# Optimization experiments

Hardware: AMD Instinct MI355X
Metric: run time of the kernel (lower is better)

## Reference

```python
import jax, jax.numpy as jnp
import numpy as np

NEG_SLOPE = 0.02

def _leaky(x):
    return jnp.where(x >= 0, x, NEG_SLOPE * x)

def _conv1d(x, w, b):
    # x: (B, Cin, T), w: (Cout, Cin, 3) torch layout; SAME padding, stride 1
    y = jax.lax.conv_general_dilated(x, w, window_strides=(1,), padding=[(1, 1)],
                                     dimension_numbers=('NCH', 'OIH', 'NCH'))
    return y + b[None, :, None]

def setup_inputs() -> dict:
    key = jax.random.key(0)
    ks = iter(jax.random.split(key, 40))
    B, T, NA, S, NE, NID = 32768, 9, 64, 32, 53, 5000
    def rn(shape, scale=0.1):
        return (jax.random.normal(next(ks), shape, dtype=jnp.float32) * scale)
    inp = {
        'x': jax.random.normal(next(ks), (B, T, NA), dtype=jnp.float32),
        'identity_id': jax.random.randint(next(ks), (B,), 0, NID, dtype=jnp.int32),
        'cw1': rn((32, 64, 3)), 'cb1': rn((32,)),
        'cw2': rn((64, 32, 3)), 'cb2': rn((64,)),
        'cw3': rn((128, 64, 3)), 'cb3': rn((128,)),
        'cw4': rn((64, 128, 3)), 'cb4': rn((64,)),
        'fw1': rn((128, 64)), 'fb1': rn((128,)),
        'fw2': rn((64, 128)), 'fb2': rn((64,)),
        'fw3': rn((32, 64)), 'fb3': rn((32,)),
        'aw1': rn((16, 32, 3)), 'ab1': rn((16,)),
        'aw2': rn((8, 16, 3)), 'ab2': rn((8,)),
        'aw3': rn((4, 8, 3)), 'ab3': rn((4,)),
        'aw4': rn((2, 4, 3)), 'ab4': rn((2,)),
        'aw5': rn((1, 2, 3)), 'ab5': rn((1,)),
        'lw': rn((9, 9)), 'lb': rn((9,)),
        'mapping': jax.random.normal(next(ks), (1, NID, NE, S), dtype=jnp.float32),
    }
    return inp

def reference(x, identity_id, cw1, cb1, cw2, cb2, cw3, cb3, cw4, cb4,
              fw1, fb1, fw2, fb2, fw3, fb3,
              aw1, ab1, aw2, ab2, aw3, ab3, aw4, ab4, aw5, ab5,
              lw, lb, mapping):
    B, T, _ = x.shape          # (B, 9, 64)
    S = fw3.shape[0]           # subspace_dim = 32
    h = jnp.transpose(x, (0, 2, 1))  # (B, 64, 9)
    h = _leaky(_conv1d(h, cw1, cb1))
    h = _leaky(_conv1d(h, cw2, cb2))
    h = _leaky(_conv1d(h, cw3, cb3))
    h = _leaky(_conv1d(h, cw4, cb4))  # (B, 64, 9)
    # faithful to torch: reshape (B,64,9) -> (B*9, 1, 64) row-major (mixes C and T)
    h = h.reshape(B * T, 64)
    h = _leaky(h @ fw1.T + fb1)
    h = _leaky(h @ fw2.T + fb2)
    h = jnp.tanh(h @ fw3.T + fb3)        # (B*T, S)
    rs_T = h.reshape(B, T, S).transpose(0, 2, 1)  # (B, S, T)
    a = _leaky(_conv1d(rs_T, aw1, ab1))
    a = _leaky(_conv1d(a, aw2, ab2))
    a = _leaky(_conv1d(a, aw3, ab3))
    a = _leaky(_conv1d(a, aw4, ab4))
    a = _leaky(_conv1d(a, aw5, ab5))     # (B, 1, T)
    logits = a.reshape(B, T) @ lw.T + lb
    att = jax.nn.softmax(logits, axis=1)            # (B, T)
    sub = jnp.einsum('bst,bt->bs', rs_T, att)       # (B, S)
    m = mapping[0][identity_id]                     # (B, n_expression, S)
    return 10.0 * jnp.einsum('bes,bs->be', m, sub)  # (B, n_expression)
```

## Files before the change

### kernel.cpp

```cpp
#include <hip/hip_runtime.h>
#include <hip/hip_bf16.h>
#include <math.h>

#define THREADS 512
#define WAVES 8
#define NB 16

typedef __attribute__((ext_vector_type(8))) short bf16x8;
typedef __attribute__((ext_vector_type(4))) float f32x4;

__device__ __forceinline__ float leaky(float x){ return x >= 0.f ? x : 0.02f*x; }
__device__ __forceinline__ float fast_tanh(float x){
  float e = __expf(2.f*x);
  return 1.f - 2.f/(e + 1.f);
}

__device__ __forceinline__ unsigned short f2bf(float f){
  union { float f; unsigned u; } v; v.f = f;
  unsigned r = (v.u + 0x7FFFu + ((v.u >> 16) & 1u)) >> 16;
  return (unsigned short)r;
}
__device__ __forceinline__ float bf2f(unsigned short h){
  union { unsigned u; float f; } v; v.u = ((unsigned)h) << 16;
  return v.f;
}
__device__ __forceinline__ unsigned pack2bf(float a, float b){
  float2 t; t.x = a; t.y = b;
  __hip_bfloat162 h = __float22bfloat162_rn(t);
  union { __hip_bfloat162 h; unsigned u; } c; c.h = h;
  return c.u;
}

template<int L2R>
__device__ __forceinline__ unsigned swz(unsigned b){
  if constexpr (L2R < 0) return b;
  else return b ^ (((b >> L2R) & 7u) << 4);
}

__device__ __forceinline__ f32x4 mfma16(bf16x8 a, bf16x8 b, f32x4 c){
  return __builtin_amdgcn_mfma_f32_16x16x32_bf16(a, b, c, 0, 0, 0);
}

#define WB_C1 0
#define WB_C2 6144
#define WB_C3 12288
#define WB_C4 36864
#define WB_F1 61440
#define WB_F2 69632
#define WB_F3 77824
#define WB_A1 79872
#define WB_A2 81408
#define WB_A3 82432
#define WB_A4 82944
#define WB_A5 83456
#define WP_TOTAL 83968

__global__ void pack_weights(
    const float* __restrict__ cw1, const float* __restrict__ cw2,
    const float* __restrict__ cw3, const float* __restrict__ cw4,
    const float* __restrict__ fw1, const float* __restrict__ fw2,
    const float* __restrict__ fw3, const float* __restrict__ aw1,
    const float* __restrict__ aw2, const float* __restrict__ aw3,
    const float* __restrict__ aw4, const float* __restrict__ aw5,
    short* __restrict__ wp)
{
  int g = blockIdx.x*256 + threadIdx.x;
  if (g >= WP_TOTAL) return;
  const float* w; int base, l2cp, cinw, cout, KS; bool conv;
  if      (g < WB_C2){ w=cw1; base=WB_C1; l2cp=6; cinw=64;  cout=32;  KS=6;  conv=true; }
  else if (g < WB_C3){ w=cw2; base=WB_C2; l2cp=5; cinw=32;  cout=64;  KS=3;  conv=true; }
  else if (g < WB_C4){ w=cw3; base=WB_C3; l2cp=6; cinw=64;  cout=128; KS=6;  conv=true; }
  else if (g < WB_F1){ w=cw4; base=WB_C4; l2cp=7; cinw=128; cout=64;  KS=12; conv=true; }
  else if (g < WB_F2){ w=fw1; base=WB_F1; l2cp=6; cinw=64;  cout=128; KS=2;  conv=false; }
  else if (g < WB_F3){ w=fw2; base=WB_F2; l2cp=7; cinw=128; cout=64;  KS=4;  conv=false; }
  else if (g < WB_A1){ w=fw3; base=WB_F3; l2cp=6; cinw=64;  cout=32;  KS=2;  conv=false; }
  else if (g < WB_A2){ w=aw1; base=WB_A1; l2cp=5; cinw=32;  cout=16;  KS=3;  conv=true; }
  else if (g < WB_A3){ w=aw2; base=WB_A2; l2cp=4; cinw=16;  cout=8;   KS=2;  conv=true; }
  else if (g < WB_A4){ w=aw3; base=WB_A3; l2cp=3; cinw=8;   cout=4;   KS=1;  conv=true; }
  else if (g < WB_A5){ w=aw4; base=WB_A4; l2cp=3; cinw=4;   cout=2;   KS=1;  conv=true; }
  else               { w=aw5; base=WB_A5; l2cp=3; cinw=2;   cout=1;   KS=1;  conv=true; }
  int local = g - base;
  int frag = local >> 9;
  int lane = (local >> 3) & 63;
  int j    = local & 7;
  int nt = frag / KS, ks = frag - nt*KS;
  int hi = lane >> 4, lo = lane & 15;
  int k = ks*32 + hi*8 + j;
  int n = nt*16 + lo;
  float v = 0.f;
  if (n < cout){
    if (conv){
      int dt = k >> l2cp, ci = k & ((1<<l2cp)-1);
      if (dt < 3 && ci < cinw) v = w[((size_t)n*cinw + ci)*3 + dt];
    } else {
      v = w[(size_t)n*cinw + k];
    }
  }
  wp[g] = (short)f2bf(v);
}

template<int CINP, int CINW, int COUT, int STORE_CH, int KS, int MYNT,
         int L2RI, int L2RO, bool IN_CONV, int OUT_MODE, int ACT,
         int LBASE, bool PACKED>
__device__ __forceinline__ void mfma_layer(
    const short* __restrict__ wp, const float* __restrict__ w,
    const float* __restrict__ bias, const char* __restrict__ inb,
    char* __restrict__ outb, int tid)
{
  constexpr int NT = (COUT + 15)/16;
  constexpr int NTG = (NT + MYNT - 1)/MYNT;
  constexpr int L2CINP = (CINP==8?3:CINP==16?4:CINP==32?5:CINP==64?6:7);
  const int wave = tid >> 6, lane = tid & 63;
  const int hi = lane >> 4, lo = lane & 15;

  int nt0, mlo, mhi;
  if constexpr (NTG >= WAVES){
    nt0 = (wave % NTG) * MYNT; mlo = 0; mhi = 9;
  } else {
    constexpr int WPN = WAVES/NTG;
    int seg = wave / NTG; int g = wave - seg*NTG;
    nt0 = g*MYNT; mlo = (9*seg)/WPN; mhi = (9*(seg+1))/WPN;
  }

  bf16x8 Bf[MYNT][KS];
  #pragma unroll
  for (int nt = 0; nt < MYNT; ++nt){
    #pragma unroll
    for (int ks = 0; ks < KS; ++ks){
      if constexpr (PACKED){
        Bf[nt][ks] = *(const bf16x8*)(wp + LBASE + (((nt0+nt)*KS + ks) << 9) + lane*8);
      } else {
        int n = (nt0+nt)*16 + lo;
        #pragma unroll
        for (int j = 0; j < 8; ++j){
          int k = ks*32 + hi*8 + j;
          float v = 0.f;
          if (n < COUT){
            if constexpr (IN_CONV){
              int dt = k >> L2CINP, ci = k & (CINP-1);
              if (dt < 3 && ci < CINW) v = w[((size_t)n*CINW + ci)*3 + dt];
            } else {
              v = w[(size_t)n*CINP + k];
            }
          }
          Bf[nt][ks][j] = (short)f2bf(v);
        }
      }
    }
  }

  float bb[MYNT][4];
  #pragma unroll
  for (int nt = 0; nt < MYNT; ++nt){
    #pragma unroll
    for (int r = 0; r < 4; ++r){
      int n = (nt0+nt)*16 + hi*4 + r;
      bb[nt][r] = (n < COUT) ? bias[n] : 0.f;
    }
  }

  const unsigned hi16 = (unsigned)hi * 16u;

  for (int m = mlo; m < mhi; ++m){
    int R = m*16 + lo;
    int bl2 = 0, t2 = 0, ridx = R;
    if constexpr (IN_CONV || OUT_MODE != 1){
      bl2 = R/9; t2 = R - bl2*9; ridx = bl2*11 + t2;
    }
    unsigned base_in;
    if constexpr (IN_CONV) base_in = ((unsigned)ridx << (L2CINP+1));
    else                   base_in = ((unsigned)R    << (L2CINP+1));

    f32x4 acc[MYNT];
    #pragma unroll
    for (int nt = 0; nt < MYNT; ++nt)
      acc[nt] = (f32x4){bb[nt][0], bb[nt][1], bb[nt][2], bb[nt][3]};

    #pragma unroll
    for (int ks = 0; ks < KS; ++ks){
      unsigned byte0 = base_in + (unsigned)(ks*64) + hi16;
      bf16x8 Af = *(const bf16x8*)(inb + swz<L2RI>(byte0));
      #pragma unroll
      for (int nt = 0; nt < MYNT; ++nt)
        acc[nt] = mfma16(Bf[nt][ks], Af, acc[nt]);
    }

    #pragma unroll
    for (int nt = 0; nt < MYNT; ++nt){
      const int n0 = (nt0+nt)*16 + hi*4;
      if constexpr (OUT_MODE == 2){
        #pragma unroll
        for (int r = 0; r < 4; ++r){
          int n = n0 + r;
          float vr = (ACT==0) ? leaky(acc[nt][r]) : fast_tanh(acc[nt][r]);
          unsigned byte = (unsigned)((bl2*576 + n*9 + t2)*2);
          *(short*)(outb + swz<L2RO>(byte)) = (short)f2bf(vr);
        }
      } else if constexpr (STORE_CH == 1){
        if (hi == 0){
          float vr = (ACT==0) ? leaky(acc[nt][0]) : fast_tanh(acc[nt][0]);
          *(short*)(outb + (unsigned)((ridx + 1)*2)) = (short)f2bf(vr);
        }
      } else {
        if (n0 < STORE_CH){
          float v[4];
          #pragma unroll
          for (int r = 0; r < 4; ++r){
            float vr = (ACT==0) ? leaky(acc[nt][r]) : fast_tanh(acc[nt][r]);
            if constexpr (STORE_CH > COUT){ if (n0 + r >= COUT) vr = 0.f; }
            v[r] = vr;
          }
          unsigned rowO = (OUT_MODE == 1) ? (unsigned)R : (unsigned)(ridx + 1);
          unsigned byte = rowO * (unsigned)(STORE_CH*2) + (unsigned)(n0*2);
          uint2 pk; pk.x = pack2bf(v[0], v[1]); pk.y = pack2bf(v[2], v[3]);
          *(uint2*)(outb + swz<L2RO>(byte)) = pk;
        }
      }
    }
  }

  if constexpr (OUT_MODE == 0){
    for (int i = tid; i < NB*2*STORE_CH/4; i += THREADS){
      int bl = i / (2*STORE_CH/4); int rem = i - bl*(2*STORE_CH/4);
      int side = rem / (STORE_CH/4); int c4 = rem - side*(STORE_CH/4);
      unsigned byte = (unsigned)(((bl*11 + side*10)*STORE_CH + c4*4)*2);
      uint2 z; z.x = 0u; z.y = 0u;
      *(uint2*)(outb + swz<L2RO>(byte)) = z;
    }
  }
}

#define A2OFF 5760
#define A3OFF 8704
#define A4OFF 11648
#define A5OFF 14592

template<bool PACKED>
__global__ __launch_bounds__(THREADS, 4)
void fused_expr_kernel(
    const float* __restrict__ x, const int* __restrict__ ident,
    const float* __restrict__ cw1, const float* __restrict__ cb1,
    const float* __restrict__ cw2, const float* __restrict__ cb2,
    const float* __restrict__ cw3, const float* __restrict__ cb3,
    const float* __restrict__ cw4, const float* __restrict__ cb4,
    const float* __restrict__ fw1, const float* __restrict__ fb1,
    const float* __restrict__ fw2, const float* __restrict__ fb2,
    const float* __restrict__ fw3, const float* __restrict__ fb3,
    const float* __restrict__ aw1, const float* __restrict__ ab1,
    const float* __restrict__ aw2, const float* __restrict__ ab2,
    const float* __restrict__ aw3, const float* __restrict__ ab3,
    const float* __restrict__ aw4, const float* __restrict__ ab4,
    const float* __restrict__ aw5, const float* __restrict__ ab5,
    const float* __restrict__ lw,  const float* __restrict__ lb,
    const float* __restrict__ mapping, const short* __restrict__ wp,
    float* __restrict__ out)
{
  __shared__ __align__(16) char pool[67584];
  __shared__ float logits_s[NB*9];
  __shared__ float att_s[NB*9];
  __shared__ float sub_s[NB*32];

  char* RA = pool;
  char* RB = pool + 45056;

  const int tid = threadIdx.x;
  const int b0 = blockIdx.x * NB;
  const int p  = tid >> 4;
  const int bl = tid & 15;

  {
    const float4* xb4 = (const float4*)(x + (size_t)b0 * 576);
    for (int i = tid; i < NB*144; i += THREADS){
      int b = i / 144; int rem = i - b*144;
      int t = rem >> 4; int c4 = rem & 15;
      float4 v = xb4[i];
      uint2 pk;
      pk.x = pack2bf(v.x, v.y);
      pk.y = pack2bf(v.z, v.w);
      unsigned byte = (unsigned)(((b*11 + t + 1)*64 + c4*4)*2);
      *(uint2*)(RB + swz<7>(byte)) = pk;
    }
    for (int i = tid; i < 512; i += THREADS){
      int b = i >> 5; int rem = i & 31;
      int side = rem >> 4; int c4 = rem & 15;
      unsigned byte = (unsigned)(((b*11 + side*10)*64 + c4*4)*2);
      uint2 z; z.x = 0u; z.y = 0u;
      *(uint2*)(RB + swz<7>(byte)) = z;
    }
  }
  __syncthreads();

  mfma_layer<64, 64, 32, 32, 6, 2, 7, 6, true, 0, 0, WB_C1, PACKED>(wp, cw1, cb1, RB, RA, tid); __syncthreads();
  mfma_layer<32, 32, 64, 64, 3, 2, 6, 7, true, 0, 0, WB_C2, PACKED>(wp, cw2, cb2, RA, RB, tid); __syncthreads();
  mfma_layer<64, 64,128,128, 6, 2, 7, 8, true, 0, 0, WB_C3, PACKED>(wp, cw3, cb3, RB, RA, tid); __syncthreads();
  mfma_layer<128,128,64, 64,12, 1, 8, 7, true, 2, 0, WB_C4, PACKED>(wp, cw4, cb4, RA, RB, tid); __syncthreads();
  mfma_layer<64, 64,128,128, 2, 4, 7, 8, false,1, 0, WB_F1, PACKED>(wp, fw1, fb1, RB, RA, tid); __syncthreads();
  mfma_layer<128,128,64, 64, 4, 2, 8, 7, false,1, 0, WB_F2, PACKED>(wp, fw2, fb2, RA, RB, tid); __syncthreads();
  mfma_layer<64, 64, 32, 32, 2, 2, 7, 6, false,0, 1, WB_F3, PACKED>(wp, fw3, fb3, RB, RA, tid); __syncthreads();

  char* rs = RA;
  char* a1 = RB;
  char* a2 = RB + A2OFF;
  char* a3 = RB + A3OFF;
  char* a4 = RB + A4OFF;
  char* a5 = RB + A5OFF;

  mfma_layer<32, 32, 16, 16, 3, 1, 6, 5, true, 0, 0, WB_A1, PACKED>(wp, aw1, ab1, rs, a1, tid); __syncthreads();
  mfma_layer<16, 16,  8,  8, 2, 1, 5,-1, true, 0, 0, WB_A2, PACKED>(wp, aw2, ab2, a1, a2, tid); __syncthreads();
  mfma_layer< 8,  8,  4,  8, 1, 1,-1,-1, true, 0, 0, WB_A3, PACKED>(wp, aw3, ab3, a2, a3, tid); __syncthreads();
  mfma_layer< 8,  4,  2,  8, 1, 1,-1,-1, true, 0, 0, WB_A4, PACKED>(wp, aw4, ab4, a3, a4, tid); __syncthreads();
  mfma_layer< 8,  2,  1,  1, 1, 1,-1,-1, true, 3, 0, WB_A5, PACKED>(wp, aw5, ab5, a4, a5, tid); __syncthreads();

  if (p < 9){
    float acc = lb[p];
    #pragma unroll
    for (int t = 0; t < 9; ++t)
      acc = fmaf(lw[p*9 + t], bf2f(*(const unsigned short*)(a5 + (bl*11 + t + 1)*2)), acc);
    logits_s[bl*9 + p] = acc;
  }
  __syncthreads();

  if (p == 0){
    float m = -1e30f;
    #pragma unroll
    for (int t = 0; t < 9; ++t) m = fmaxf(m, logits_s[bl*9 + t]);
    float s = 0.f, ex[9];
    #pragma unroll
    for (int t = 0; t < 9; ++t){ ex[t] = __expf(logits_s[bl*9 + t] - m); s += ex[t]; }
    float inv = 1.f / s;
    #pragma unroll
    for (int t = 0; t < 9; ++t) att_s[bl*9 + t] = ex[t]*inv;
  }
  __syncthreads();

  {
    int s = p;
    float acc = 0.f;
    #pragma unroll
    for (int t = 0; t < 9; ++t){
      unsigned byte = (unsigned)(((bl*11 + t + 1)*32 + s)*2);
      acc = fmaf(bf2f(*(const unsigned short*)(rs + swz<6>(byte))), att_s[bl*9 + t], acc);
    }
    sub_s[bl*32 + s] = acc;
  }
  __syncthreads();

  {
    const int b = b0 + bl;
    const size_t id = (size_t)ident[b];
    const float* mb = mapping + id*53*32;
    float subv[32];
    #pragma unroll
    for (int s = 0; s < 32; ++s) subv[s] = sub_s[bl*32 + s];
    for (int e = p; e < 53; e += 32){
      const float4* mrow4 = (const float4*)(mb + e*32);
      float acc = 0.f;
      #pragma unroll
      for (int s4 = 0; s4 < 8; ++s4){
        float4 mv = mrow4[s4];
        acc = fmaf(mv.x, subv[s4*4+0], acc);
        acc = fmaf(mv.y, subv[s4*4+1], acc);
        acc = fmaf(mv.z, subv[s4*4+2], acc);
        acc = fmaf(mv.w, subv[s4*4+3], acc);
      }
      out[(size_t)b*53 + e] = 10.f*acc;
    }
  }
}

extern "C" void kernel_launch(void* const* d_in, const int* in_sizes, int n_in,
                              void* d_out, int out_size, void* d_ws, size_t ws_size,
                              hipStream_t stream) {
  const float* x    = (const float*)d_in[0];
  const int*   ident= (const int*)  d_in[1];
  const float* cw1  = (const float*)d_in[2];  const float* cb1 = (const float*)d_in[3];
  const float* cw2  = (const float*)d_in[4];  const float* cb2 = (const float*)d_in[5];
  const float* cw3  = (const float*)d_in[6];  const float* cb3 = (const float*)d_in[7];
  const float* cw4  = (const float*)d_in[8];  const float* cb4 = (const float*)d_in[9];
  const float* fw1  = (const float*)d_in[10]; const float* fb1 = (const float*)d_in[11];
  const float* fw2  = (const float*)d_in[12]; const float* fb2 = (const float*)d_in[13];
  const float* fw3  = (const float*)d_in[14]; const float* fb3 = (const float*)d_in[15];
  const float* aw1  = (const float*)d_in[16]; const float* ab1 = (const float*)d_in[17];
  const float* aw2  = (const float*)d_in[18]; const float* ab2 = (const float*)d_in[19];
  const float* aw3  = (const float*)d_in[20]; const float* ab3 = (const float*)d_in[21];
  const float* aw4  = (const float*)d_in[22]; const float* ab4 = (const float*)d_in[23];
  const float* aw5  = (const float*)d_in[24]; const float* ab5 = (const float*)d_in[25];
  const float* lw   = (const float*)d_in[26]; const float* lb  = (const float*)d_in[27];
  const float* mapping = (const float*)d_in[28];

  const int B = 32768;
  dim3 grid(B / NB), block(THREADS);

  const bool packed = ws_size >= (size_t)(WP_TOTAL * 2);
  short* wpk = (short*)d_ws;

  if (packed){
    pack_weights<<<dim3(WP_TOTAL/256), dim3(256), 0, stream>>>(
        cw1, cw2, cw3, cw4, fw1, fw2, fw3, aw1, aw2, aw3, aw4, aw5, wpk);
    fused_expr_kernel<true><<<grid, block, 0, stream>>>(
        x, ident, cw1, cb1, cw2, cb2, cw3, cb3, cw4, cb4,
        fw1, fb1, fw2, fb2, fw3, fb3,
        aw1, ab1, aw2, ab2, aw3, ab3, aw4, ab4, aw5, ab5,
        lw, lb, mapping, wpk, (float*)d_out);
  } else {
    fused_expr_kernel<false><<<grid, block, 0, stream>>>(
        x, ident, cw1, cb1, cw2, cb2, cw3, cb3, cw4, cb4,
        fw1, fb1, fw2, fb2, fw3, fb3,
        aw1, ab1, aw2, ab2, aw3, ab3, aw4, ab4, aw5, ab5,
        lw, lb, mapping, wpk, (float*)d_out);
  }
}
```

Baseline: 145.5 us.

## Halve batch per block, drop padded rows, and raise occupancy

Each block now handles 8 sequences instead of 16, and activations are stored densely (9 rows per sequence) rather than with padding rows. Conv boundaries are handled by masked A-fragment loads instead of explicitly zeroing pad rows. The shared-memory pool shrinks from about 66KB to about 30KB, and launch bounds now target 8 blocks per SM, so more blocks fit per CU. In exchange, per-tile MYNT drops to 1 in several layers, so each block reloads weights more often relative to its work, and the conditional loads add branches to the inner loop.

Measured after the change: 269.9 us. +85.5%, slower.

```diff
diff --git a/kernel.cpp b/kernel.cpp
--- a/kernel.cpp
+++ b/kernel.cpp
@@ -4,7 +4,14 @@
 
 #define THREADS 512
 #define WAVES 8
-#define NB 16
+#define NB 8
+#define MROWS (NB*9)
+#define MT 5
+
+#define P1OFF 0
+#define P2OFF 20480
+#define GUARD 256
+#define POOLSZ (20480+10240+GUARD)
 
 typedef __attribute__((ext_vector_type(8))) short bf16x8;
 typedef __attribute__((ext_vector_type(4))) float f32x4;
@@ -115,11 +122,11 @@
 
   int nt0, mlo, mhi;
   if constexpr (NTG >= WAVES){
-    nt0 = (wave % NTG) * MYNT; mlo = 0; mhi = 9;
+    nt0 = (wave % NTG)*MYNT; mlo = 0; mhi = MT;
   } else {
     constexpr int WPN = WAVES/NTG;
     int seg = wave / NTG; int g = wave - seg*NTG;
-    nt0 = g*MYNT; mlo = (9*seg)/WPN; mhi = (9*(seg+1))/WPN;
+    nt0 = g*MYNT; mlo = (MT*seg)/WPN; mhi = (MT*(seg+1))/WPN;
   }
 
   bf16x8 Bf[MYNT][KS];
@@ -159,17 +166,15 @@
     }
   }
 
-  const unsigned hi16 = (unsigned)hi * 16u;
+  const int k0h = hi*8;
 
   for (int m = mlo; m < mhi; ++m){
     int R = m*16 + lo;
-    int bl2 = 0, t2 = 0, ridx = R;
-    if constexpr (IN_CONV || OUT_MODE != 1){
-      bl2 = R/9; t2 = R - bl2*9; ridx = bl2*11 + t2;
-    }
-    unsigned base_in;
-    if constexpr (IN_CONV) base_in = ((unsigned)ridx << (L2CINP+1));
-    else                   base_in = ((unsigned)R    << (L2CINP+1));
+    int tl = 0;
+    if constexpr (IN_CONV){
+      int blr = (int)((unsigned)R/9u);
+      tl = R - blr*9;
+    }
 
     f32x4 acc[MYNT];
     #pragma unroll
@@ -178,8 +183,18 @@
 
     #pragma unroll
     for (int ks = 0; ks < KS; ++ks){
-      unsigned byte0 = base_in + (unsigned)(ks*64) + hi16;
-      bf16x8 Af = *(const bf16x8*)(inb + swz<L2RI>(byte0));
+      bf16x8 Af = {};
+      if constexpr (IN_CONV){
+        int k0 = ks*32 + k0h;
+        int dtv = k0 >> L2CINP;
+        if ((unsigned)(tl + dtv - 1) < 9u && dtv < 3){
+          unsigned byte0 = (unsigned)(((R-1) << (L2CINP+1)) + (k0 << 1));
+          Af = *(const bf16x8*)(inb + swz<L2RI>(byte0));
+        }
+      } else {
+        unsigned byte0 = (unsigned)((R << (L2CINP+1)) + (ks*32 + k0h)*2);
+        Af = *(const bf16x8*)(inb + swz<L2RI>(byte0));
+      }
       #pragma unroll
       for (int nt = 0; nt < MYNT; ++nt)
         acc[nt] = mfma16(Bf[nt][ks], Af, acc[nt]);
@@ -189,17 +204,19 @@
     for (int nt = 0; nt < MYNT; ++nt){
       const int n0 = (nt0+nt)*16 + hi*4;
       if constexpr (OUT_MODE == 2){
-        #pragma unroll
-        for (int r = 0; r < 4; ++r){
-          int n = n0 + r;
-          float vr = (ACT==0) ? leaky(acc[nt][r]) : fast_tanh(acc[nt][r]);
-          unsigned byte = (unsigned)((bl2*576 + n*9 + t2)*2);
-          *(short*)(outb + swz<L2RO>(byte)) = (short)f2bf(vr);
+        if (R < MROWS){
+          int blr = (int)((unsigned)R/9u); int t2 = R - blr*9;
+          #pragma unroll
+          for (int r = 0; r < 4; ++r){
+            float vr = leaky(acc[nt][r]);
+            unsigned byte = (unsigned)((blr*576 + (n0+r)*9 + t2)*2);
+            *(short*)(outb + swz<L2RO>(byte)) = (short)f2bf(vr);
+          }
         }
-      } else if constexpr (STORE_CH == 1){
+      } else if constexpr (OUT_MODE == 3){
         if (hi == 0){
           float vr = (ACT==0) ? leaky(acc[nt][0]) : fast_tanh(acc[nt][0]);
-          *(short*)(outb + (unsigned)((ridx + 1)*2)) = (short)f2bf(vr);
+          *(short*)(outb + (unsigned)(R*2)) = (short)f2bf(vr);
         }
       } else {
         if (n0 < STORE_CH){
@@ -210,33 +227,17 @@
             if constexpr (STORE_CH > COUT){ if (n0 + r >= COUT) vr = 0.f; }
             v[r] = vr;
           }
-          unsigned rowO = (OUT_MODE == 1) ? (unsigned)R : (unsigned)(ridx + 1);
-          unsigned byte = rowO * (unsigned)(STORE_CH*2) + (unsigned)(n0*2);
+          unsigned byte = (unsigned)R*(unsigned)(STORE_CH*2) + (unsigned)(n0*2);
           uint2 pk; pk.x = pack2bf(v[0], v[1]); pk.y = pack2bf(v[2], v[3]);
           *(uint2*)(outb + swz<L2RO>(byte)) = pk;
         }
       }
     }
   }
-
-  if constexpr (OUT_MODE == 0){
-    for (int i = tid; i < NB*2*STORE_CH/4; i += THREADS){
-      int bl = i / (2*STORE_CH/4); int rem = i - bl*(2*STORE_CH/4);
-      int side = rem / (STORE_CH/4); int c4 = rem - side*(STORE_CH/4);
-      unsigned byte = (unsigned)(((bl*11 + side*10)*STORE_CH + c4*4)*2);
-      uint2 z; z.x = 0u; z.y = 0u;
-      *(uint2*)(outb + swz<L2RO>(byte)) = z;
-    }
-  }
-}
-
-#define A2OFF 5760
-#define A3OFF 8704
-#define A4OFF 11648
-#define A5OFF 14592
+}
 
 template<bool PACKED>
-__global__ __launch_bounds__(THREADS, 4)
+__global__ __launch_bounds__(THREADS, 8)
 void fused_expr_kernel(
     const float* __restrict__ x, const int* __restrict__ ident,
     const float* __restrict__ cw1, const float* __restrict__ cb1,
@@ -255,18 +256,18 @@
     const float* __restrict__ mapping, const short* __restrict__ wp,
     float* __restrict__ out)
 {
-  __shared__ __align__(16) char pool[67584];
+  __shared__ __align__(16) char pool[POOLSZ];
   __shared__ float logits_s[NB*9];
   __shared__ float att_s[NB*9];
   __shared__ float sub_s[NB*32];
 
-  char* RA = pool;
-  char* RB = pool + 45056;
+  char* P1 = pool + P1OFF;
+  char* P2 = pool + P2OFF;
 
   const int tid = threadIdx.x;
   const int b0 = blockIdx.x * NB;
-  const int p  = tid >> 4;
-  const int bl = tid & 15;
+  const int p  = tid >> 3;
+  const int bl = tid & 7;
 
   {
     const float4* xb4 = (const float4*)(x + (size_t)b0 * 576);
@@ -277,33 +278,32 @@
       uint2 pk;
       pk.x = pack2bf(v.x, v.y);
       pk.y = pack2bf(v.z, v.w);
-      unsigned byte = (unsigned)(((b*11 + t + 1)*64 + c4*4)*2);
-      *(uint2*)(RB + swz<7>(byte)) = pk;
-    }
-    for (int i = tid; i < 512; i += THREADS){
-      int b = i >> 5; int rem = i & 31;
-      int side = rem >> 4; int c4 = rem & 15;
-      unsigned byte = (unsigned)(((b*11 + side*10)*64 + c4*4)*2);
+      unsigned byte = (unsigned)(((b*9 + t)*64 + c4*4)*2);
+      *(uint2*)(P2 + swz<7>(byte)) = pk;
+    }
+    for (int i = tid; i < 128; i += THREADS){
+      int rr = 72 + (i >> 4); int c4 = i & 15;
+      unsigned byte = (unsigned)((rr*64 + c4*4)*2);
       uint2 z; z.x = 0u; z.y = 0u;
-      *(uint2*)(RB + swz<7>(byte)) = z;
+      *(uint2*)(P2 + swz<7>(byte)) = z;
     }
   }
   __syncthreads();
 
-  mfma_layer<64, 64, 32, 32, 6, 2, 7, 6, true, 0, 0, WB_C1, PACKED>(wp, cw1, cb1, RB, RA, tid); __syncthreads();
-  mfma_layer<32, 32, 64, 64, 3, 2, 6, 7, true, 0, 0, WB_C2, PACKED>(wp, cw2, cb2, RA, RB, tid); __syncthreads();
-  mfma_layer<64, 64,128,128, 6, 2, 7, 8, true, 0, 0, WB_C3, PACKED>(wp, cw3, cb3, RB, RA, tid); __syncthreads();
-  mfma_layer<128,128,64, 64,12, 1, 8, 7, true, 2, 0, WB_C4, PACKED>(wp, cw4, cb4, RA, RB, tid); __syncthreads();
-  mfma_layer<64, 64,128,128, 2, 4, 7, 8, false,1, 0, WB_F1, PACKED>(wp, fw1, fb1, RB, RA, tid); __syncthreads();
-  mfma_layer<128,128,64, 64, 4, 2, 8, 7, false,1, 0, WB_F2, PACKED>(wp, fw2, fb2, RA, RB, tid); __syncthreads();
-  mfma_layer<64, 64, 32, 32, 2, 2, 7, 6, false,0, 1, WB_F3, PACKED>(wp, fw3, fb3, RB, RA, tid); __syncthreads();
-
-  char* rs = RA;
-  char* a1 = RB;
-  char* a2 = RB + A2OFF;
-  char* a3 = RB + A3OFF;
-  char* a4 = RB + A4OFF;
-  char* a5 = RB + A5OFF;
+  mfma_layer<64, 64, 32, 32, 6, 1, 7, 6, true, 0, 0, WB_C1, PACKED>(wp, cw1, cb1, P2, P1, tid); __syncthreads();
+  mfma_layer<32, 32, 64, 64, 3, 1, 6, 7, true, 0, 0, WB_C2, PACKED>(wp, cw2, cb2, P1, P2, tid); __syncthreads();
+  mfma_layer<64, 64,128,128, 6, 1, 7, 8, true, 0, 0, WB_C3, PACKED>(wp, cw3, cb3, P2, P1, tid); __syncthreads();
+  mfma_layer<128,128,64, 64,12, 1, 8, 7, true, 2, 0, WB_C4, PACKED>(wp, cw4, cb4, P1, P2, tid); __syncthreads();
+  mfma_layer<64, 64,128,128, 2, 2, 7, 8, false,0, 0, WB_F1, PACKED>(wp, fw1, fb1, P2, P1, tid); __syncthreads();
+  mfma_layer<128,128,64, 64, 4, 1, 8, 7, false,0, 0, WB_F2, PACKED>(wp, fw2, fb2, P1, P2, tid); __syncthreads();
+  mfma_layer<64, 64, 32, 32, 2, 1, 7, 6, false,0, 1, WB_F3, PACKED>(wp, fw3, fb3, P2, P1, tid); __syncthreads();
+
+  char* rs = P1;
+  char* a1 = P2;
+  char* a2 = P1 + 8192;
+  char* a3 = P2 + 4096;
+  char* a4 = P1 + 10240;
+  char* a5 = P2 + 6144;
 
   mfma_layer<32, 32, 16, 16, 3, 1, 6, 5, true, 0, 0, WB_A1, PACKED>(wp, aw1, ab1, rs, a1, tid); __syncthreads();
   mfma_layer<16, 16,  8,  8, 2, 1, 5,-1, true, 0, 0, WB_A2, PACKED>(wp, aw2, ab2, a1, a2, tid); __syncthreads();
@@ -315,7 +315,7 @@
     float acc = lb[p];
     #pragma unroll
     for (int t = 0; t < 9; ++t)
-      acc = fmaf(lw[p*9 + t], bf2f(*(const unsigned short*)(a5 + (bl*11 + t + 1)*2)), acc);
+      acc = fmaf(lw[p*9 + t], bf2f(*(const unsigned short*)(a5 + (bl*9 + t)*2)), acc);
     logits_s[bl*9 + p] = acc;
   }
   __syncthreads();
@@ -333,12 +333,12 @@
   }
   __syncthreads();
 
-  {
+  if (p < 32){
     int s = p;
     float acc = 0.f;
     #pragma unroll
     for (int t = 0; t < 9; ++t){
-      unsigned byte = (unsigned)(((bl*11 + t + 1)*32 + s)*2);
+      unsigned byte = (unsigned)(((bl*9 + t)*32 + s)*2);
       acc = fmaf(bf2f(*(const unsigned short*)(rs + swz<6>(byte))), att_s[bl*9 + t], acc);
     }
     sub_s[bl*32 + s] = acc;
@@ -352,8 +352,8 @@
     float subv[32];
     #pragma unroll
     for (int s = 0; s < 32; ++s) subv[s] = sub_s[bl*32 + s];
-    for (int e = p; e < 53; e += 32){
-      const float4* mrow4 = (const float4*)(mb + e*32);
+    if (p < 53){
+      const float4* mrow4 = (const float4*)(mb + p*32);
       float acc = 0.f;
       #pragma unroll
       for (int s4 = 0; s4 < 8; ++s4){
@@ -363,7 +363,7 @@
         acc = fmaf(mv.z, subv[s4*4+2], acc);
         acc = fmaf(mv.w, subv[s4*4+3], acc);
       }
-      out[(size_t)b*53 + e] = 10.f*acc;
+      out[(size_t)b*53 + p] = 10.f*acc;
     }
   }
 }
```
